# Kernel tuning notes

Hardware: AMD Instinct MI355X
Metric: run time of the kernel (lower is better)

The kernel has to match this reference:

```python
import jax, jax.numpy as jnp
import numpy as np

D = 128      # dims[0]: number of nodes
M1 = 256     # dims[1]
M2 = 128     # dims[2]
M3 = 1       # dims[3] (must be 1 for final squeeze)
B = 4096     # batch


def setup_inputs() -> dict:
    key = jax.random.key(0)
    ks = jax.random.split(key, 7)
    x = jax.random.normal(ks[0], (B, D), dtype=jnp.float32)
    # nn.Linear(D, D*M1): weight [D*M1, D], bias [D*M1]
    bnd1 = 1.0 / np.sqrt(D)
    W1 = jax.random.uniform(ks[1], (D * M1, D), minval=-bnd1, maxval=bnd1, dtype=jnp.float32)
    b1 = jax.random.uniform(ks[2], (D * M1,), minval=-bnd1, maxval=bnd1, dtype=jnp.float32)
    # An(D, M1, M2): weight [D, M1, M2], bias [D, M2]
    bnd_a = 1.0 / np.sqrt(M1)
    Wa = jax.random.uniform(ks[3], (D, M1, M2), minval=-bnd_a, maxval=bnd_a, dtype=jnp.float32)
    ba = jax.random.uniform(ks[4], (D, M2), minval=-bnd_a, maxval=bnd_a, dtype=jnp.float32)
    # An(D, M2, M3): weight [D, M2, M3], bias [D, M3]
    bnd_b = 1.0 / np.sqrt(M2)
    Wb = jax.random.uniform(ks[5], (D, M2, M3), minval=-bnd_b, maxval=bnd_b, dtype=jnp.float32)
    bb = jax.random.uniform(ks[6], (D, M3), minval=-bnd_b, maxval=bnd_b, dtype=jnp.float32)
    return {"x": x, "W1": W1, "b1": b1, "Wa": Wa, "ba": ba, "Wb": Wb, "bb": bb}


def reference(x, W1, b1, Wa, ba, Wb, bb):
    # a1: [B, D] -> [B, D*M1] -> [B, D, M1]
    h = (x @ W1.T + b1).reshape(B, D, M1)
    # An layer 1: sigmoid then per-node matmul + bias
    h = jnp.einsum('bni,nio->bno', jax.nn.sigmoid(h), Wa) + ba  # [B, D, M2]
    # An layer 2
    h = jnp.einsum('bni,nio->bno', jax.nn.sigmoid(h), Wb) + bb  # [B, D, 1]
    return h.squeeze(axis=2)  # [B, D]
```

## Files before the change

kernel.cpp:

```cpp
#include <hip/hip_runtime.h>

#define D_NODES 128
#define KD      128
#define M1_     256
#define M2_     128
#define B_      4096
#define BM      256
#define WROWS   32
#define CI      64
#define NCH     4

typedef short bf16x8  __attribute__((ext_vector_type(8)));
typedef short short4v __attribute__((ext_vector_type(4)));
typedef float f32x4   __attribute__((ext_vector_type(4)));

#define MFMA16(a, b, c) __builtin_amdgcn_mfma_f32_16x16x32_bf16((a), (b), (c), 0, 0, 0)

__device__ __forceinline__ short f2b(float f) {
  unsigned u = __builtin_bit_cast(unsigned, f);
  u += 0x7FFFu + ((u >> 16) & 1u);
  return (short)(u >> 16);
}

__device__ __forceinline__ float sigmoidf_(float x) {
  float e = __builtin_amdgcn_exp2f(-1.44269504088896f * x);
  return __builtin_amdgcn_rcpf(1.0f + e);
}

__global__ void cvt_f2b_k(const float* __restrict__ in, short* __restrict__ out) {
  int i = (blockIdx.x * 256 + threadIdx.x) * 4;
  float4 f = *(const float4*)(in + i);
  short4v s; s[0] = f2b(f.x); s[1] = f2b(f.y); s[2] = f2b(f.z); s[3] = f2b(f.w);
  *(short4v*)(out + i) = s;
}

__global__ void trans_wa_k(const float* __restrict__ Wa, short* __restrict__ waT) {
  __shared__ float lt[64][129];
  int node = blockIdx.x >> 2, iblk = blockIdx.x & 3;
  int t = threadIdx.x;
  for (int j = 0; j < 32; ++j) {
    int e = j * 256 + t;
    int i = e >> 7, o = e & 127;
    lt[i][o] = Wa[(node * M1_ + iblk * 64 + i) * M2_ + o];
  }
  __syncthreads();
  int il = t & 63, ob = t >> 6;
  for (int j = 0; j < 32; ++j) {
    int o = j * 4 + ob;
    waT[(node * M2_ + o) * M1_ + iblk * 64 + il] = f2b(lt[il][o]);
  }
}

template <bool FAST>
__global__ __launch_bounds__(512, 2)
void fused_dag_k(const float* __restrict__ x,  const float* __restrict__ W1,
                 const float* __restrict__ b1, const float* __restrict__ Wa,
                 const float* __restrict__ ba, const float* __restrict__ Wb,
                 const float* __restrict__ bb, float* __restrict__ out,
                 const short* __restrict__ w1b, const short* __restrict__ waT,
                 const short* __restrict__ xb) {
  __shared__ __align__(16) short w1s[M1_ * KD];
  __shared__ __align__(16) short was[M2_ * M1_];
  __shared__ __align__(16) short h1w[8 * 16 * CI];

  int gid = blockIdx.x;
  int xcd = gid & 7, ii = gid >> 3;
  int node = xcd * 16 + (ii >> 4);
  int tile = ii & 15;
  int b0 = tile * BM;

  int t = threadIdx.x;
  int w = t >> 6, l = t & 63;
  int n15 = l & 15, q = l >> 4;

  if (FAST) {
    const short* w1n = w1b + (size_t)node * M1_ * KD;
    const short* wan = waT + (size_t)node * M2_ * M1_;
    bf16x8 t1[8], t2[8];
#pragma unroll
    for (int j = 0; j < 8; ++j) t1[j] = *(const bf16x8*)(w1n + (j * 512 + t) * 8);
#pragma unroll
    for (int j = 0; j < 8; ++j) t2[j] = *(const bf16x8*)(wan + (j * 512 + t) * 8);
#pragma unroll
    for (int j = 0; j < 8; ++j) {
      int s = j * 512 + t;
      int row = s >> 4, g = s & 15;
      *(bf16x8*)(&w1s[row * KD + ((g ^ (row & 7)) << 3)]) = t1[j];
    }
#pragma unroll
    for (int j = 0; j < 8; ++j) {
      int s = j * 512 + t;
      int row = s >> 5, g = s & 31;
      *(bf16x8*)(&was[row * M1_ + ((g ^ (row & 7)) << 3)]) = t2[j];
    }
  } else {
#pragma unroll
    for (int j = 0; j < 8; ++j) {
      int s = j * 512 + t;
      int row = s >> 4, g = s & 15;
      const float* src = W1 + ((size_t)node * M1_ + row) * KD + g * 8;
      float4 f0 = *(const float4*)(src);
      float4 f1 = *(const float4*)(src + 4);
      bf16x8 v;
      v[0] = f2b(f0.x); v[1] = f2b(f0.y); v[2] = f2b(f0.z); v[3] = f2b(f0.w);
      v[4] = f2b(f1.x); v[5] = f2b(f1.y); v[6] = f2b(f1.z); v[7] = f2b(f1.w);
      *(bf16x8*)(&w1s[row * KD + ((g ^ (row & 7)) << 3)]) = v;
    }
    for (int j = 0; j < 8; ++j) {
      int s = j * 512 + t;
      int o = s >> 5, g = s & 31;
      bf16x8 v;
#pragma unroll
      for (int e = 0; e < 8; ++e)
        v[e] = f2b(Wa[((size_t)node * M1_ + g * 8 + e) * M2_ + o]);
      *(bf16x8*)(&was[o * M1_ + ((g ^ (o & 7)) << 3)]) = v;
    }
  }

  bf16x8 xa[2][4];
  {
    int rb = b0 + w * WROWS;
#pragma unroll
    for (int mt = 0; mt < 2; ++mt) {
      int row = rb + mt * 16 + n15;
#pragma unroll
      for (int kk = 0; kk < 4; ++kk) {
        int k0 = kk * 32 + q * 8;
        if (FAST) {
          xa[mt][kk] = *(const bf16x8*)(xb + row * KD + k0);
        } else {
          float4 f0 = *(const float4*)(x + row * KD + k0);
          float4 f1 = *(const float4*)(x + row * KD + k0 + 4);
          bf16x8 v;
          v[0] = f2b(f0.x); v[1] = f2b(f0.y); v[2] = f2b(f0.z); v[3] = f2b(f0.w);
          v[4] = f2b(f1.x); v[5] = f2b(f1.y); v[6] = f2b(f1.z); v[7] = f2b(f1.w);
          xa[mt][kk] = v;
        }
      }
    }
  }

  __syncthreads();

  f32x4 acc2[2][8];
#pragma unroll
  for (int a = 0; a < 2; ++a)
#pragma unroll
    for (int b = 0; b < 8; ++b) acc2[a][b] = (f32x4){0.f, 0.f, 0.f, 0.f};

  short* myh1 = &h1w[w * 16 * CI];
  int swz = n15 & 7;

  for (int c = 0; c < NCH; ++c) {
    f32x4 acc1[4][2];
#pragma unroll
    for (int a = 0; a < 4; ++a)
#pragma unroll
      for (int b = 0; b < 2; ++b) acc1[a][b] = (f32x4){0.f, 0.f, 0.f, 0.f};
#pragma unroll
    for (int kk = 0; kk < 4; ++kk) {
      int gsw = (4 * kk + q) ^ swz;
#pragma unroll
      for (int it = 0; it < 4; ++it) {
        int row = c * CI + it * 16 + n15;
        bf16x8 wf = *(const bf16x8*)(&w1s[row * KD + (gsw << 3)]);
        acc1[it][0] = MFMA16(wf, xa[0][kk], acc1[it][0]);
        acc1[it][1] = MFMA16(wf, xa[1][kk], acc1[it][1]);
      }
    }

    bf16x8 wa[8][2];
#pragma unroll
    for (int ot = 0; ot < 8; ++ot) {
      int o = ot * 16 + n15;
#pragma unroll
      for (int kk = 0; kk < 2; ++kk) {
        int g = (c * 8 + kk * 4 + q) ^ swz;
        wa[ot][kk] = *(const bf16x8*)(&was[o * M1_ + (g << 3)]);
      }
    }

    const float* b1c = b1 + node * M1_ + c * CI;
#pragma unroll
    for (int mt = 0; mt < 2; ++mt) {
#pragma unroll
      for (int it = 0; it < 4; ++it) {
        f32x4 bv = *(const f32x4*)(b1c + it * 16 + q * 4);
        short4v s4;
#pragma unroll
        for (int r = 0; r < 4; ++r)
          s4[r] = f2b(sigmoidf_(acc1[it][mt][r] + bv[r]));
        int gi = (2 * it + (q >> 1)) ^ swz;
        *(short4v*)(&myh1[n15 * CI + (gi << 3) + (q & 1) * 4]) = s4;
      }
#pragma unroll
      for (int kk = 0; kk < 2; ++kk) {
        int g = (4 * kk + q) ^ swz;
        bf16x8 ha = *(const bf16x8*)(&myh1[n15 * CI + (g << 3)]);
#pragma unroll
        for (int ot = 0; ot < 8; ++ot)
          acc2[mt][ot] = MFMA16(ha, wa[ot][kk], acc2[mt][ot]);
      }
    }
  }

  const float* ban = ba + node * M2_;
  const float* wbn = Wb + node * M2_;
  float bbv = bb[node];
#pragma unroll
  for (int mt = 0; mt < 2; ++mt) {
    f32x4 rs = (f32x4){0.f, 0.f, 0.f, 0.f};
#pragma unroll
    for (int ot = 0; ot < 8; ++ot) {
      int o = ot * 16 + n15;
      float bav = ban[o];
      float wbv = wbn[o];
#pragma unroll
      for (int r = 0; r < 4; ++r)
        rs[r] += sigmoidf_(acc2[mt][ot][r] + bav) * wbv;
    }
#pragma unroll
    for (int r = 0; r < 4; ++r) {
      float v = rs[r];
      v += __shfl_xor(v, 1);
      v += __shfl_xor(v, 2);
      v += __shfl_xor(v, 4);
      v += __shfl_xor(v, 8);
      if (n15 == 0)
        out[(size_t)(b0 + w * WROWS + mt * 16 + q * 4 + r) * D_NODES + node] = v + bbv;
    }
  }
}

extern "C" void kernel_launch(void* const* d_in, const int* in_sizes, int n_in,
                              void* d_out, int out_size, void* d_ws, size_t ws_size,
                              hipStream_t stream) {
  const float* x  = (const float*)d_in[0];
  const float* W1 = (const float*)d_in[1];
  const float* b1 = (const float*)d_in[2];
  const float* Wa = (const float*)d_in[3];
  const float* ba = (const float*)d_in[4];
  const float* Wb = (const float*)d_in[5];
  const float* bb = (const float*)d_in[6];
  float* out = (float*)d_out;

  const size_t W1_ELEMS = (size_t)D_NODES * M1_ * KD;
  const size_t WA_ELEMS = (size_t)D_NODES * M1_ * M2_;
  const size_t X_ELEMS  = (size_t)B_ * KD;
  const size_t NEED = (W1_ELEMS + WA_ELEMS + X_ELEMS) * sizeof(short);

  const int GRID = D_NODES * (B_ / BM);

  if (ws_size >= NEED) {
    short* w1b = (short*)d_ws;
    short* waT = w1b + W1_ELEMS;
    short* xb  = waT + WA_ELEMS;
    cvt_f2b_k<<<(int)(W1_ELEMS / 1024), 256, 0, stream>>>(W1, w1b);
    cvt_f2b_k<<<(int)(X_ELEMS / 1024), 256, 0, stream>>>(x, xb);
    trans_wa_k<<<D_NODES * 4, 256, 0, stream>>>(Wa, waT);
    fused_dag_k<true><<<GRID, 512, 0, stream>>>(x, W1, b1, Wa, ba, Wb, bb, out, w1b, waT, xb);
  } else {
    fused_dag_k<false><<<GRID, 512, 0, stream>>>(x, W1, b1, Wa, ba, Wb, bb, out,
                                                 nullptr, nullptr, nullptr);
  }
}
```

Before: 128.5 us.

## Stream Wa fragments from global into registers instead of staging in LDS

Drops the 64 KB shared-memory copy of the transposed Wa tile. Each chunk now loads its Wa MFMA fragments straight from global memory (L2-resident bf16 waT) into registers. This halves LDS use per block, so more blocks may fit per CU, and removes the upfront staging. The cost is repeated global loads per wave and chunk, whose latency may be exposed. The sigmoid bias is also folded into an FMA with a pre-scaled bias.

```diff
diff --git a/kernel.cpp b/kernel.cpp
--- a/kernel.cpp
+++ b/kernel.cpp
@@ -6,9 +6,9 @@
 #define M2_     128
 #define B_      4096
 #define BM      256
-#define WROWS   32
 #define CI      64
 #define NCH     4
+#define LOG2E   1.44269504088896f
 
 typedef short bf16x8  __attribute__((ext_vector_type(8)));
 typedef short short4v __attribute__((ext_vector_type(4)));
@@ -22,8 +22,9 @@
   return (short)(u >> 16);
 }
 
-__device__ __forceinline__ float sigmoidf_(float x) {
-  float e = __builtin_amdgcn_exp2f(-1.44269504088896f * x);
+__device__ __forceinline__ float sigmoid_pre(float acc, float bs) {
+  float tt = __builtin_fmaf(acc, -LOG2E, bs);
+  float e = __builtin_amdgcn_exp2f(tt);
   return __builtin_amdgcn_rcpf(1.0f + e);
 }
 
@@ -60,7 +61,6 @@
                  const short* __restrict__ w1b, const short* __restrict__ waT,
                  const short* __restrict__ xb) {
   __shared__ __align__(16) short w1s[M1_ * KD];
-  __shared__ __align__(16) short was[M2_ * M1_];
   __shared__ __align__(16) short h1w[8 * 16 * CI];
 
   int gid = blockIdx.x;
@@ -72,26 +72,18 @@
   int t = threadIdx.x;
   int w = t >> 6, l = t & 63;
   int n15 = l & 15, q = l >> 4;
+  int swz = n15 & 7;
 
   if (FAST) {
-    const short* w1n = w1b + (size_t)node * M1_ * KD;
-    const short* wan = waT + (size_t)node * M2_ * M1_;
-    bf16x8 t1[8], t2[8];
+    const short* w1n = w1b + (size_t)node * (M1_ * KD);
+    bf16x8 t1[8];
 #pragma unroll
     for (int j = 0; j < 8; ++j) t1[j] = *(const bf16x8*)(w1n + (j * 512 + t) * 8);
-#pragma unroll
-    for (int j = 0; j < 8; ++j) t2[j] = *(const bf16x8*)(wan + (j * 512 + t) * 8);
 #pragma unroll
     for (int j = 0; j < 8; ++j) {
       int s = j * 512 + t;
       int row = s >> 4, g = s & 15;
       *(bf16x8*)(&w1s[row * KD + ((g ^ (row & 7)) << 3)]) = t1[j];
-    }
-#pragma unroll
-    for (int j = 0; j < 8; ++j) {
-      int s = j * 512 + t;
-      int row = s >> 5, g = s & 31;
-      *(bf16x8*)(&was[row * M1_ + ((g ^ (row & 7)) << 3)]) = t2[j];
     }
   } else {
 #pragma unroll
@@ -106,20 +98,11 @@
       v[4] = f2b(f1.x); v[5] = f2b(f1.y); v[6] = f2b(f1.z); v[7] = f2b(f1.w);
       *(bf16x8*)(&w1s[row * KD + ((g ^ (row & 7)) << 3)]) = v;
     }
-    for (int j = 0; j < 8; ++j) {
-      int s = j * 512 + t;
-      int o = s >> 5, g = s & 31;
-      bf16x8 v;
-#pragma unroll
-      for (int e = 0; e < 8; ++e)
-        v[e] = f2b(Wa[((size_t)node * M1_ + g * 8 + e) * M2_ + o]);
-      *(bf16x8*)(&was[o * M1_ + ((g ^ (o & 7)) << 3)]) = v;
-    }
   }
 
   bf16x8 xa[2][4];
   {
-    int rb = b0 + w * WROWS;
+    int rb = b0 + w * 32;
 #pragma unroll
     for (int mt = 0; mt < 2; ++mt) {
       int row = rb + mt * 16 + n15;
@@ -149,14 +132,33 @@
     for (int b = 0; b < 8; ++b) acc2[a][b] = (f32x4){0.f, 0.f, 0.f, 0.f};
 
   short* myh1 = &h1w[w * 16 * CI];
-  int swz = n15 & 7;
+  const short* wan = waT + (size_t)node * (M2_ * M1_);
+  bf16x8 wa[8][2];
 
   for (int c = 0; c < NCH; ++c) {
+#pragma unroll
+    for (int ot = 0; ot < 8; ++ot)
+#pragma unroll
+      for (int kk = 0; kk < 2; ++kk) {
+        if (FAST) {
+          wa[ot][kk] =
+              *(const bf16x8*)(wan + (ot * 16 + n15) * M1_ + c * CI + kk * 32 + q * 8);
+        } else {
+          bf16x8 v;
+#pragma unroll
+          for (int e = 0; e < 8; ++e)
+            v[e] = f2b(Wa[((size_t)node * M1_ + c * CI + kk * 32 + q * 8 + e) * M2_ +
+                          (ot * 16 + n15)]);
+          wa[ot][kk] = v;
+        }
+      }
+
     f32x4 acc1[4][2];
 #pragma unroll
-    for (int a = 0; a < 4; ++a)
-#pragma unroll
-      for (int b = 0; b < 2; ++b) acc1[a][b] = (f32x4){0.f, 0.f, 0.f, 0.f};
+    for (int a = 0; a < 4; ++a) {
+      acc1[a][0] = (f32x4){0.f, 0.f, 0.f, 0.f};
+      acc1[a][1] = (f32x4){0.f, 0.f, 0.f, 0.f};
+    }
 #pragma unroll
     for (int kk = 0; kk < 4; ++kk) {
       int gsw = (4 * kk + q) ^ swz;
@@ -169,27 +171,17 @@
       }
     }
 
-    bf16x8 wa[8][2];
-#pragma unroll
-    for (int ot = 0; ot < 8; ++ot) {
-      int o = ot * 16 + n15;
-#pragma unroll
-      for (int kk = 0; kk < 2; ++kk) {
-        int g = (c * 8 + kk * 4 + q) ^ swz;
-        wa[ot][kk] = *(const bf16x8*)(&was[o * M1_ + (g << 3)]);
-      }
-    }
-
     const float* b1c = b1 + node * M1_ + c * CI;
 #pragma unroll
     for (int mt = 0; mt < 2; ++mt) {
 #pragma unroll
       for (int it = 0; it < 4; ++it) {
         f32x4 bv = *(const f32x4*)(b1c + it * 16 + q * 4);
+        f32x4 bs = bv * (-LOG2E);
         short4v s4;
 #pragma unroll
         for (int r = 0; r < 4; ++r)
-          s4[r] = f2b(sigmoidf_(acc1[it][mt][r] + bv[r]));
+          s4[r] = f2b(sigmoid_pre(acc1[it][mt][r], bs[r]));
         int gi = (2 * it + (q >> 1)) ^ swz;
         *(short4v*)(&myh1[n15 * CI + (gi << 3) + (q & 1) * 4]) = s4;
       }
@@ -207,18 +199,21 @@
   const float* ban = ba + node * M2_;
   const float* wbn = Wb + node * M2_;
   float bbv = bb[node];
+  float bas[8], wbs[8];
+#pragma unroll
+  for (int ot = 0; ot < 8; ++ot) {
+    int o = ot * 16 + n15;
+    bas[ot] = ban[o] * (-LOG2E);
+    wbs[ot] = wbn[o];
+  }
 #pragma unroll
   for (int mt = 0; mt < 2; ++mt) {
     f32x4 rs = (f32x4){0.f, 0.f, 0.f, 0.f};
 #pragma unroll
-    for (int ot = 0; ot < 8; ++ot) {
-      int o = ot * 16 + n15;
-      float bav = ban[o];
-      float wbv = wbn[o];
+    for (int ot = 0; ot < 8; ++ot)
 #pragma unroll
       for (int r = 0; r < 4; ++r)
-        rs[r] += sigmoidf_(acc2[mt][ot][r] + bav) * wbv;
-    }
+        rs[r] += sigmoid_pre(acc2[mt][ot][r], bas[ot]) * wbs[ot];
 #pragma unroll
     for (int r = 0; r < 4; ++r) {
       float v = rs[r];
@@ -227,7 +222,7 @@
       v += __shfl_xor(v, 4);
       v += __shfl_xor(v, 8);
       if (n15 == 0)
-        out[(size_t)(b0 + w * WROWS + mt * 16 + q * 4 + r) * D_NODES + node] = v + bbv;
+        out[(size_t)(b0 + w * 32 + mt * 16 + q * 4 + r) * D_NODES + node] = v + bbv;
     }
   }
 }
@@ -258,7 +253,8 @@
     cvt_f2b_k<<<(int)(W1_ELEMS / 1024), 256, 0, stream>>>(W1, w1b);
     cvt_f2b_k<<<(int)(X_ELEMS / 1024), 256, 0, stream>>>(x, xb);
     trans_wa_k<<<D_NODES * 4, 256, 0, stream>>>(Wa, waT);
-    fused_dag_k<true><<<GRID, 512, 0, stream>>>(x, W1, b1, Wa, ba, Wb, bb, out, w1b, waT, xb);
+    fused_dag_k<true><<<GRID, 512, 0, stream>>>(x, W1, b1, Wa, ba, Wb, bb, out,
+                                                w1b, waT, xb);
   } else {
     fused_dag_k<false><<<GRID, 512, 0, stream>>>(x, W1, b1, Wa, ba, Wb, bb, out,
                                                  nullptr, nullptr, nullptr);
```

Result: slower. 187.8 us (+46.2%).
